# Optimization experiments

Hardware: AMD Instinct MI355X
Metric: run time of the kernel (lower is better)

The kernel has to match this reference:

```python
import jax, jax.numpy as jnp
import numpy as np

D_MODEL, D_FFN, N_LEVELS, N_HEADS, N_POINTS = 256, 1024, 4, 8, 4
B, LQ = 2, 8192
SHAPES = [(128, 128), (64, 64), (32, 32), (16, 16)]  # (H_l, W_l) per level
D_HEAD = D_MODEL // N_HEADS


def setup_inputs() -> dict:
    key = jax.random.key(0)
    ks = jax.random.split(key, 16)
    S = sum(h * w for h, w in SHAPES)

    def lin_w(k, fin, fout):
        s = 1.0 / np.sqrt(fin)
        return jax.random.uniform(k, (fin, fout), jnp.float32, -s, s)

    inp = {
        "tgt": jax.random.normal(ks[0], (B, LQ, D_MODEL), jnp.float32),
        "query_pos": jax.random.normal(ks[1], (B, LQ, D_MODEL), jnp.float32),
        "reference_points": jax.random.uniform(ks[2], (B, LQ, N_LEVELS, 2), jnp.float32),
        "src": jax.random.normal(ks[3], (B, S, D_MODEL), jnp.float32),
        "spatial_shapes": np.array(SHAPES, dtype=np.int64),
        "level_start_index": np.concatenate([[0], np.cumsum([h * w for h, w in SHAPES])[:-1]]).astype(np.int64),
        "W_value": lin_w(ks[4], D_MODEL, D_MODEL),
        "b_value": jnp.zeros((D_MODEL,), jnp.float32),
        "W_off": lin_w(ks[5], D_MODEL, N_HEADS * N_LEVELS * N_POINTS * 2),
        "b_off": 0.5 * jax.random.normal(ks[6], (N_HEADS * N_LEVELS * N_POINTS * 2,), jnp.float32),
        "W_attn": lin_w(ks[7], D_MODEL, N_HEADS * N_LEVELS * N_POINTS),
        "b_attn": jnp.zeros((N_HEADS * N_LEVELS * N_POINTS,), jnp.float32),
        "W_out": lin_w(ks[8], D_MODEL, D_MODEL),
        "b_out": jnp.zeros((D_MODEL,), jnp.float32),
        "ln1_g": jnp.ones((D_MODEL,), jnp.float32),
        "ln1_b": jnp.zeros((D_MODEL,), jnp.float32),
        "W1": lin_w(ks[9], D_MODEL, D_FFN),
        "b1": jnp.zeros((D_FFN,), jnp.float32),
        "W2": lin_w(ks[10], D_FFN, D_MODEL),
        "b2": jnp.zeros((D_MODEL,), jnp.float32),
        "ln3_g": jnp.ones((D_MODEL,), jnp.float32),
        "ln3_b": jnp.zeros((D_MODEL,), jnp.float32),
    }
    return inp


def _layer_norm(x, g, b, eps=1e-5):
    mu = jnp.mean(x, -1, keepdims=True)
    var = jnp.mean((x - mu) ** 2, -1, keepdims=True)
    return (x - mu) * jax.lax.rsqrt(var + eps) * g + b


def _ms_deform_attn(q, reference_points, src, shapes,
                    W_value, b_value, W_off, b_off, W_attn, b_attn, W_out, b_out):
    Bq, Lq, _ = q.shape
    value = (src @ W_value + b_value).reshape(Bq, -1, N_HEADS, D_HEAD)
    value = jnp.transpose(value, (0, 2, 1, 3))  # [B, H, S, Dh]
    off = (q @ W_off + b_off).reshape(Bq, Lq, N_HEADS, N_LEVELS, N_POINTS, 2)
    attn = jax.nn.softmax((q @ W_attn + b_attn).reshape(Bq, Lq, N_HEADS, N_LEVELS * N_POINTS), axis=-1)
    attn = attn.reshape(Bq, Lq, N_HEADS, N_LEVELS, N_POINTS)
    # offset normalizer is (W_l, H_l) per level
    normalizer = jnp.array([[w, h] for h, w in shapes], jnp.float32)
    loc = reference_points[:, :, None, :, None, :] + off / normalizer[None, None, None, :, None, :]

    out = jnp.zeros((Bq, Lq, N_HEADS, D_HEAD), jnp.float32)
    start = 0
    for l, (Hl, Wl) in enumerate(shapes):
        Nl = Hl * Wl
        v_l = value[:, :, start:start + Nl]  # [B, H, Nl, Dh]
        start += Nl
        loc_l = jnp.transpose(loc[:, :, :, l, :, :], (0, 2, 1, 3, 4))  # [B, H, Lq, P, 2]
        # grid_sample (align_corners=False, zero padding) pixel coords
        x = loc_l[..., 0] * Wl - 0.5
        y = loc_l[..., 1] * Hl - 0.5
        x0, y0 = jnp.floor(x), jnp.floor(y)
        wx, wy = x - x0, y - y0
        acc = jnp.zeros((Bq, N_HEADS, Lq, N_POINTS, D_HEAD), jnp.float32)
        for dx, dy, w in ((0, 0, (1 - wx) * (1 - wy)), (1, 0, wx * (1 - wy)),
                          (0, 1, (1 - wx) * wy), (1, 1, wx * wy)):
            xi, yi = x0 + dx, y0 + dy
            valid = (xi >= 0) & (xi < Wl) & (yi >= 0) & (yi < Hl)
            idx = (jnp.clip(yi, 0, Hl - 1) * Wl + jnp.clip(xi, 0, Wl - 1)).astype(jnp.int32)
            g = jnp.take_along_axis(v_l, idx.reshape(Bq, N_HEADS, -1, 1), axis=2)
            g = g.reshape(Bq, N_HEADS, Lq, N_POINTS, D_HEAD)
            acc = acc + jnp.where(valid[..., None], w[..., None] * g, 0.0)
        a = jnp.transpose(attn[:, :, :, l, :], (0, 2, 1, 3))  # [B, H, Lq, P]
        out = out + jnp.einsum('bhqp,bhqpd->bqhd', a, acc)
    return out.reshape(Bq, Lq, D_MODEL) @ W_out + b_out


def reference(tgt, query_pos, reference_points, src, spatial_shapes, level_start_index,
              W_value, b_value, W_off, b_off, W_attn, b_attn, W_out, b_out,
              ln1_g, ln1_b, W1, b1, W2, b2, ln3_g, ln3_b):
    shapes = [(int(h), int(w)) for h, w in np.asarray(spatial_shapes)]
    q = tgt + query_pos  # with_pos_embed
    tgt2 = _ms_deform_attn(q, reference_points, src, shapes,
                           W_value, b_value, W_off, b_off, W_attn, b_attn, W_out, b_out)
    x = _layer_norm(tgt + tgt2, ln1_g, ln1_b)  # dropout = identity (eval)
    ff = jax.nn.relu(x @ W1 + b1) @ W2 + b2
    return _layer_norm(x + ff, ln3_g, ln3_b)
```

## Files before the change

kernel.cpp:

```cpp
#include <hip/hip_runtime.h>
#include <hip/hip_bf16.h>
#include <hip/hip_fp16.h>
#include <math.h>

#define D_MODEL   256
#define D_FFN     1024
#define N_LEVELS  4
#define N_HEADS   8
#define N_POINTS  4
#define BATCH     2
#define LQ        8192
#define S_TOTAL   21760
#define M_Q       (BATCH*LQ)
#define M_V       (BATCH*S_TOTAL)
#define VTILES    (M_V/128)

typedef __attribute__((ext_vector_type(8))) short bf16x8;
typedef __attribute__((ext_vector_type(4))) float floatx4;

struct alignas(8)  bh4 { __hip_bfloat16 a, b, c, d; };
struct alignas(16) bh8 { __hip_bfloat16 v[8]; };

__device__ __forceinline__ void gld_lds16(const void* g, void* l) {
    __builtin_amdgcn_global_load_lds(
        (const __attribute__((address_space(1))) void*)g,
        (__attribute__((address_space(3))) void*)l, 16, 0, 0);
}

__device__ __forceinline__ bh4 pack4(float4 a) {
    return { __float2bfloat16(a.x), __float2bfloat16(a.y),
             __float2bfloat16(a.z), __float2bfloat16(a.w) };
}

template<int BM, int BN, int K>
__device__ __forceinline__ void gemm_core(const __hip_bfloat16* __restrict__ A,
                                          const __hip_bfloat16* __restrict__ Bt,
                                          int row0, int nb0, int lda, int ldb,
                                          short* As, short* Bs,
                                          floatx4 (&acc)[BM/64][BN/16])
{
    constexpr int NT  = BN / 16;
    constexpr int AF  = BM / 64;
    constexpr int BCH = BN / 64;
    constexpr int NIT = K / 32;

    const int tid  = threadIdx.x;
    const int w    = tid >> 6;
    const int lane = tid & 63;
    const int quad = lane >> 4;
    const int l15  = lane & 15;
    const size_t ldaB = (size_t)lda * 2, ldbB = (size_t)ldb * 2;

    const char* gA[AF]; int lA[AF];
#pragma unroll
    for (int i = 0; i < AF; i++) {
        int o = (w * AF + i) * 1024 + lane * 16;
        gA[i] = (const char*)A + (size_t)(row0 + (o >> 6)) * ldaB + (o & 63);
        lA[i] = (w * AF + i) * 512;
    }
    const char* gB[BCH]; int lB[BCH];
#pragma unroll
    for (int j = 0; j < BCH; j++) {
        int o = (w * BCH + j) * 1024 + lane * 16;
        gB[j] = (const char*)Bt + (size_t)(nb0 + (o >> 6)) * ldbB + (o & 63);
        lB[j] = (w * BCH + j) * 512;
    }

#pragma unroll
    for (int i = 0; i < AF; i++)  gld_lds16(gA[i], &As[lA[i]]);
#pragma unroll
    for (int j = 0; j < BCH; j++) gld_lds16(gB[j], &Bs[lB[j]]);

#pragma unroll 8
    for (int it = 0; it < NIT; ++it) {
        __syncthreads();
        const int cb = it & 1;
        if (it + 1 < NIT) {
            const size_t kb = (size_t)(it + 1) * 64;
            const int nb = cb ^ 1;
#pragma unroll
            for (int i = 0; i < AF; i++)  gld_lds16(gA[i] + kb, &As[nb * BM * 32 + lA[i]]);
#pragma unroll
            for (int j = 0; j < BCH; j++) gld_lds16(gB[j] + kb, &Bs[nb * BN * 32 + lB[j]]);
        }
        const short* Ab = &As[cb * BM * 32];
        const short* Bb = &Bs[cb * BN * 32];
        bf16x8 af[AF];
#pragma unroll
        for (int mi = 0; mi < AF; mi++)
            af[mi] = *(const bf16x8*)&Ab[(w * (AF * 16) + mi * 16 + l15) * 32 + quad * 8];
#pragma unroll
        for (int ni = 0; ni < NT; ni++) {
            bf16x8 bfr = *(const bf16x8*)&Bb[(ni * 16 + l15) * 32 + quad * 8];
#pragma unroll
            for (int mi = 0; mi < AF; mi++)
                acc[mi][ni] = __builtin_amdgcn_mfma_f32_16x16x32_bf16(af[mi], bfr, acc[mi][ni], 0, 0, 0);
        }
    }
}

template<int K, bool ADD>
__device__ __forceinline__ void gemm_core_cvtA(const float* __restrict__ Af,
                                               const float* __restrict__ A2f,
                                               const __hip_bfloat16* __restrict__ Bt,
                                               int row0, int nb0, int lda, int ldb,
                                               short* As, short* Bs,
                                               floatx4 (&acc)[2][8])
{
    constexpr int NIT = K / 32;
    const int tid  = threadIdx.x;
    const int w    = tid >> 6;
    const int lane = tid & 63;
    const int quad = lane >> 4;
    const int l15  = lane & 15;

    const int rA  = tid >> 3;
    const int k0  = (tid & 7) * 4;
    const float* gA  = Af + (size_t)(row0 + rA) * lda + k0;
    const float* gA2 = ADD ? (A2f + (size_t)(row0 + rA) * lda + k0) : nullptr;
    const int aoff = rA * 32 + k0;

    const size_t ldbB = (size_t)ldb * 2;
    const char* gB[2]; int lB[2];
#pragma unroll
    for (int j = 0; j < 2; j++) {
        int o = (w * 2 + j) * 1024 + lane * 16;
        gB[j] = (const char*)Bt + (size_t)(nb0 + (o >> 6)) * ldbB + (o & 63);
        lB[j] = (w * 2 + j) * 512;
    }

    float4 fv[4];
    auto loadA = [&](int kt) {
#pragma unroll
        for (int j = 0; j < 4; j++) {
            fv[j] = *(const float4*)(gA + (size_t)(j * 32) * lda + kt);
            if (ADD) {
                float4 t = *(const float4*)(gA2 + (size_t)(j * 32) * lda + kt);
                fv[j].x += t.x; fv[j].y += t.y; fv[j].z += t.z; fv[j].w += t.w;
            }
        }
    };
    auto writeA = [&](short* dstbuf) {
#pragma unroll
        for (int j = 0; j < 4; j++)
            *(bh4*)&dstbuf[j * 1024 + aoff] = pack4(fv[j]);
    };

    loadA(0);
#pragma unroll
    for (int j = 0; j < 2; j++) gld_lds16(gB[j], &Bs[lB[j]]);
    writeA(As);

#pragma unroll 8
    for (int it = 0; it < NIT; ++it) {
        __syncthreads();
        const int cb = it & 1;
        const bool more = (it + 1 < NIT);
        if (more) {
            loadA((it + 1) * 32);
#pragma unroll
            for (int j = 0; j < 2; j++)
                gld_lds16(gB[j] + (size_t)(it + 1) * 64, &Bs[(cb ^ 1) * 128 * 32 + lB[j]]);
        }
        const short* Ab = &As[cb * 128 * 32];
        const short* Bb = &Bs[cb * 128 * 32];
        bf16x8 af[2];
        af[0] = *(const bf16x8*)&Ab[(w * 32      + l15) * 32 + quad * 8];
        af[1] = *(const bf16x8*)&Ab[(w * 32 + 16 + l15) * 32 + quad * 8];
#pragma unroll
        for (int ni = 0; ni < 8; ni++) {
            bf16x8 bfr = *(const bf16x8*)&Bb[(ni * 16 + l15) * 32 + quad * 8];
            acc[0][ni] = __builtin_amdgcn_mfma_f32_16x16x32_bf16(af[0], bfr, acc[0][ni], 0, 0, 0);
            acc[1][ni] = __builtin_amdgcn_mfma_f32_16x16x32_bf16(af[1], bfr, acc[1][ni], 0, 0, 0);
        }
        if (more) writeA(&As[(cb ^ 1) * 128 * 32]);
    }
}

template<int BM, int BN, int K, int EPI>
__global__ __launch_bounds__(256)
void mfma_gemm(const __hip_bfloat16* __restrict__ A,
               const __hip_bfloat16* __restrict__ Bt,
               const float* __restrict__ bias,
               float* __restrict__ outf, __hip_bfloat16* __restrict__ outb,
               int lda, int ldb, int ldOut)
{
    constexpr int NT = BN / 16, AF = BM / 64;
    __shared__ alignas(16) short As[2 * BM * 32];
    __shared__ alignas(16) short Bs[2 * BN * 32];

    const int tid = threadIdx.x, w = tid >> 6, lane = tid & 63;
    const int quad = lane >> 4, l15 = lane & 15;
    const int row0 = blockIdx.x * BM, nb0 = blockIdx.y * BN;

    floatx4 acc[AF][NT];
#pragma unroll
    for (int mi = 0; mi < AF; mi++)
#pragma unroll
        for (int ni = 0; ni < NT; ni++) acc[mi][ni] = (floatx4){0.f, 0.f, 0.f, 0.f};

    gemm_core<BM, BN, K>(A, Bt, row0, nb0, lda, ldb, As, Bs, acc);

    float bias_c[NT];
#pragma unroll
    for (int ni = 0; ni < NT; ni++) bias_c[ni] = bias ? bias[nb0 + ni * 16 + l15] : 0.f;

#pragma unroll
    for (int mi = 0; mi < AF; mi++)
#pragma unroll
        for (int r = 0; r < 4; r++) {
            int row = row0 + w * (AF * 16) + mi * 16 + quad * 4 + r;
            size_t rb = (size_t)row * ldOut + nb0;
#pragma unroll
            for (int ni = 0; ni < NT; ni++) {
                float v = acc[mi][ni][r] + bias_c[ni];
                if (EPI == 2)      outb[rb + ni * 16 + l15] = __float2bfloat16(fmaxf(v, 0.f));
                else if (EPI == 1) outb[rb + ni * 16 + l15] = __float2bfloat16(v);
                else               outf[rb + ni * 16 + l15] = v;
            }
        }
}

__global__ __launch_bounds__(256)
void mfma_gemm_vq(const float* __restrict__ src,
                  const __hip_bfloat16* __restrict__ Wvt,
                  const float* __restrict__ b_value,
                  __hip_bfloat16* __restrict__ valueb,
                  const float* __restrict__ tgt, const float* __restrict__ qpos,
                  const __hip_bfloat16* __restrict__ Woat,
                  const float* __restrict__ b_off, const float* __restrict__ b_attn,
                  float* __restrict__ offb, float* __restrict__ attnb)
{
    __shared__ alignas(16) short As[2 * 128 * 32];
    __shared__ alignas(16) short Bs[2 * 128 * 32];

    const bool isV = blockIdx.x < VTILES;
    if (isV && blockIdx.y == 2) return;

    const int tid = threadIdx.x, w = tid >> 6, lane = tid & 63;
    const int quad = lane >> 4, l15 = lane & 15;
    const int nb0 = blockIdx.y * 128;

    floatx4 acc[2][8];
#pragma unroll
    for (int mi = 0; mi < 2; mi++)
#pragma unroll
        for (int ni = 0; ni < 8; ni++) acc[mi][ni] = (floatx4){0.f, 0.f, 0.f, 0.f};

    if (isV) {
        const int row0 = blockIdx.x * 128;
        gemm_core_cvtA<256, false>(src, nullptr, Wvt, row0, nb0, 256, 256, As, Bs, acc);
        float bias_c[8];
#pragma unroll
        for (int ni = 0; ni < 8; ni++) bias_c[ni] = b_value[nb0 + ni * 16 + l15];
#pragma unroll
        for (int mi = 0; mi < 2; mi++)
#pragma unroll
            for (int r = 0; r < 4; r++) {
                int row = row0 + w * 32 + mi * 16 + quad * 4 + r;
                size_t rb = (size_t)row * 256 + nb0;
#pragma unroll
                for (int ni = 0; ni < 8; ni++)
                    valueb[rb + ni * 16 + l15] = __float2bfloat16(acc[mi][ni][r] + bias_c[ni]);
            }
        return;
    }

    const int row0 = (blockIdx.x - VTILES) * 128;
    gemm_core_cvtA<256, true>(tgt, qpos, Woat, row0, nb0, 256, 256, As, Bs, acc);

    if (blockIdx.y < 2) {
        float bias_c[8];
#pragma unroll
        for (int ni = 0; ni < 8; ni++) bias_c[ni] = b_off[nb0 + ni * 16 + l15];
#pragma unroll
        for (int mi = 0; mi < 2; mi++)
#pragma unroll
            for (int r = 0; r < 4; r++) {
                int row = row0 + w * 32 + mi * 16 + quad * 4 + r;
                size_t rb = (size_t)row * 256 + nb0;
#pragma unroll
                for (int ni = 0; ni < 8; ni++)
                    offb[rb + ni * 16 + l15] = acc[mi][ni][r] + bias_c[ni];
            }
    } else {
        float bias_c[8];
#pragma unroll
        for (int ni = 0; ni < 8; ni++) bias_c[ni] = b_attn[ni * 16 + l15];
#pragma unroll
        for (int mi = 0; mi < 2; mi++)
#pragma unroll
            for (int r = 0; r < 4; r++) {
                int row = row0 + w * 32 + mi * 16 + quad * 4 + r;
                size_t rb = (size_t)row * 128;
#pragma unroll
                for (int ni = 0; ni < 8; ni++) {
                    float v = acc[mi][ni][r] + bias_c[ni];
                    float m = v;
#pragma unroll
                    for (int msk = 1; msk <= 8; msk <<= 1) m = fmaxf(m, __shfl_xor(m, msk));
                    float e = __expf(v - m);
                    float ssum = e;
#pragma unroll
                    for (int msk = 1; msk <= 8; msk <<= 1) ssum += __shfl_xor(ssum, msk);
                    attnb[rb + ni * 16 + l15] = e / ssum;
                }
            }
    }
}

template<bool B1>
__global__ __launch_bounds__(256)
void ln_kernel(const float* __restrict__ in1f, const __hip_bfloat16* __restrict__ in1b,
               const float* __restrict__ resid, const float* __restrict__ bias,
               const float* __restrict__ g, const float* __restrict__ b,
               float* __restrict__ outf, __hip_bfloat16* __restrict__ outb)
{
    const int row  = blockIdx.x * 4 + (threadIdx.x >> 6);
    const int lane = threadIdx.x & 63;
    const size_t rb = (size_t)row * 256 + lane * 4;

    float4 v = *(const float4*)(resid + rb);
    if (B1) {
        bh4 a = *(const bh4*)(in1b + rb);
        v.x += __bfloat162float(a.a); v.y += __bfloat162float(a.b);
        v.z += __bfloat162float(a.c); v.w += __bfloat162float(a.d);
    } else {
        float4 a = *(const float4*)(in1f + rb);
        v.x += a.x; v.y += a.y; v.z += a.z; v.w += a.w;
    }
    if (bias) {
        float4 c = *(const float4*)(bias + lane * 4);
        v.x += c.x; v.y += c.y; v.z += c.z; v.w += c.w;
    }
    float s  = v.x + v.y + v.z + v.w;
    float sq = v.x * v.x + v.y * v.y + v.z * v.z + v.w * v.w;
#pragma unroll
    for (int msk = 1; msk <= 32; msk <<= 1) {
        s += __shfl_xor(s, msk); sq += __shfl_xor(sq, msk);
    }
    float mean = s * (1.f / 256.f);
    float var  = sq * (1.f / 256.f) - mean * mean;
    float rstd = rsqrtf(var + 1e-5f);
    float4 gg = *(const float4*)(g + lane * 4);
    float4 bb = *(const float4*)(b + lane * 4);
    float4 o;
    o.x = (v.x - mean) * rstd * gg.x + bb.x;
    o.y = (v.y - mean) * rstd * gg.y + bb.y;
    o.z = (v.z - mean) * rstd * gg.z + bb.z;
    o.w = (v.w - mean) * rstd * gg.w + bb.w;
    *(float4*)(outf + rb) = o;
    if (outb)
        *(bh4*)(outb + rb) = { __float2bfloat16(o.x), __float2bfloat16(o.y),
                               __float2bfloat16(o.z), __float2bfloat16(o.w) };
}

__global__ __launch_bounds__(256)
void prep_kernel(const float* w0, const float* w1, const float* w2,
                 const float* w3, const float* w4, const float* w5,
                 __hip_bfloat16* o0, __hip_bfloat16* o1, __hip_bfloat16* o2,
                 __hip_bfloat16* o3, __hip_bfloat16* o4, __hip_bfloat16* o5)
{
    int t = blockIdx.x;
    const float* s; __hip_bfloat16* dst; int Kd, Nd, tl;
    if      (t < 64)  { s = w0; dst = o0; Kd = 256;  Nd = 256;  tl = t; }
    else if (t < 128) { s = w1; dst = o1; Kd = 256;  Nd = 256;  tl = t - 64; }
    else if (t < 160) { s = w2; dst = o2; Kd = 256;  Nd = 128;  tl = t - 128; }
    else if (t < 224) { s = w3; dst = o3; Kd = 256;  Nd = 256;  tl = t - 160; }
    else if (t < 480) { s = w4; dst = o4; Kd = 256;  Nd = 1024; tl = t - 224; }
    else              { s = w5; dst = o5; Kd = 1024; Nd = 256;  tl = t - 480; }
    int ntn = Nd >> 5;
    int kt = tl / ntn, nt = tl - kt * ntn;
    __shared__ float T[32][33];
    int tx = threadIdx.x & 31, ty = threadIdx.x >> 5;
#pragma unroll
    for (int i = 0; i < 4; i++) {
        int k = kt * 32 + ty + i * 8;
        T[tx][ty + i * 8] = s[(size_t)k * Nd + nt * 32 + tx];
    }
    __syncthreads();
#pragma unroll
    for (int i = 0; i < 4; i++) {
        int n = nt * 32 + ty + i * 8;
        dst[(size_t)n * Kd + kt * 32 + tx] = __float2bfloat16(T[ty + i * 8][tx]);
    }
}

#define QB 8
__global__ __launch_bounds__(256, 4)
void sample_kernel(const float* __restrict__ refp, const float* __restrict__ offb,
                   const float* __restrict__ attn,
                   const __hip_bfloat16* __restrict__ value,
                   __hip_bfloat16* __restrict__ tgt2)
{
    __shared__ unsigned spk[64 * 65];

    const int q0  = blockIdx.x * QB;
    const int tid = threadIdx.x;

#pragma unroll
    for (int k = 0; k < 4; k++) {
        const int it = tid + k * 256;
        const int ql = it >> 7, h = (it >> 4) & 7, lp = it & 15;
        const int l = lp >> 2, p = lp & 3;
        const int q = q0 + ql, b = q >> 13;
        const int Wl = 128 >> l;
        const int LST = (l == 0) ? 0 : (l == 1) ? 16384 : (l == 2) ? 20480 : 21504;

        const float rx = refp[((size_t)q * N_LEVELS + l) * 2 + 0];
        const float ry = refp[((size_t)q * N_LEVELS + l) * 2 + 1];
        const float ox = offb[(size_t)q * 256 + h * 32 + l * 8 + p * 2 + 0];
        const float oy = offb[(size_t)q * 256 + h * 32 + l * 8 + p * 2 + 1];
        const float a  = attn[(size_t)q * 128 + h * 16 + lp];

        const float x = rx * Wl - 0.5f + ox;
        const float y = ry * Wl - 0.5f + oy;
        const float x0f = floorf(x), y0f = floorf(y);
        const float wx = x - x0f, wy = y - y0f;
        const int ix = (int)x0f, iy = (int)y0f;
        const int base = b * S_TOTAL + LST;
        const int g = ql * 8 + h;
        const float cw[4] = {(1.f - wx) * (1.f - wy) * a, wx * (1.f - wy) * a,
                             (1.f - wx) * wy * a,         wx * wy * a};
#pragma unroll
        for (int c = 0; c < 4; c++) {
            const int xi = ix + (c & 1), yi = iy + (c >> 1);
            const bool valid = ((unsigned)xi < (unsigned)Wl) && ((unsigned)yi < (unsigned)Wl);
            const unsigned pix = valid ? (unsigned)(base + yi * Wl + xi) : (unsigned)base;
            const __half hw = __float2half(valid ? cw[c] : 0.f);
            spk[(lp * 4 + c) * 65 + g] = (pix << 16) | (unsigned)__half_as_ushort(hw);
        }
    }
    __syncthreads();

    const int ql = tid >> 5, h = (tid >> 2) & 7, d4 = tid & 3;
    const int q = q0 + ql, g = ql * 8 + h;
    const int c0 = h * 32 + d4 * 8;
    const char* vb = (const char*)value + (size_t)c0 * 2;

    float ac[8] = {0.f, 0.f, 0.f, 0.f, 0.f, 0.f, 0.f, 0.f};
#pragma unroll
    for (int ch = 0; ch < 4; ch++) {
        unsigned us[16];
#pragma unroll
        for (int j = 0; j < 16; j++) us[j] = spk[(ch * 16 + j) * 65 + g];
        uint4 rv[16];
#pragma unroll
        for (int j = 0; j < 16; j++)
            rv[j] = *(const uint4*)(vb + ((size_t)(us[j] >> 16) << 9));
#pragma unroll
        for (int j = 0; j < 16; j++) {
            float wv = __half2float(__ushort_as_half((unsigned short)(us[j] & 0xffffu)));
            ac[0] += wv * __uint_as_float(rv[j].x << 16);
            ac[1] += wv * __uint_as_float(rv[j].x & 0xffff0000u);
            ac[2] += wv * __uint_as_float(rv[j].y << 16);
            ac[3] += wv * __uint_as_float(rv[j].y & 0xffff0000u);
            ac[4] += wv * __uint_as_float(rv[j].z << 16);
            ac[5] += wv * __uint_as_float(rv[j].z & 0xffff0000u);
            ac[6] += wv * __uint_as_float(rv[j].w << 16);
            ac[7] += wv * __uint_as_float(rv[j].w & 0xffff0000u);
        }
    }
    bh8 o;
#pragma unroll
    for (int i = 0; i < 8; i++) o.v[i] = __float2bfloat16(ac[i]);
    *(bh8*)(tgt2 + (size_t)q * 256 + c0) = o;
}

extern "C" void kernel_launch(void* const* d_in, const int* in_sizes, int n_in,
                              void* d_out, int out_size, void* d_ws, size_t ws_size,
                              hipStream_t stream) {
    const float* tgt     = (const float*)d_in[0];
    const float* qpos    = (const float*)d_in[1];
    const float* refp    = (const float*)d_in[2];
    const float* src     = (const float*)d_in[3];
    const float* W_value = (const float*)d_in[6];
    const float* b_value = (const float*)d_in[7];
    const float* W_off   = (const float*)d_in[8];
    const float* b_off   = (const float*)d_in[9];
    const float* W_attn  = (const float*)d_in[10];
    const float* b_attn  = (const float*)d_in[11];
    const float* W_out   = (const float*)d_in[12];
    const float* b_out   = (const float*)d_in[13];
    const float* ln1_g   = (const float*)d_in[14];
    const float* ln1_b   = (const float*)d_in[15];
    const float* W1      = (const float*)d_in[16];
    const float* b1      = (const float*)d_in[17];
    const float* W2      = (const float*)d_in[18];
    const float* b2      = (const float*)d_in[19];
    const float* ln3_g   = (const float*)d_in[20];
    const float* ln3_b   = (const float*)d_in[21];
    float* out = (float*)d_out;

    char* p = (char*)d_ws;
    auto nxt = [&](size_t b) { char* r = p; p += (b + 255) & ~(size_t)255; return r; };
    __hip_bfloat16* Wvt    = (__hip_bfloat16*)nxt((size_t)256 * 256 * 2);
    __hip_bfloat16* Woat   = (__hip_bfloat16*)nxt((size_t)384 * 256 * 2);
    __hip_bfloat16* Woutt  = (__hip_bfloat16*)nxt((size_t)256 * 256 * 2);
    __hip_bfloat16* W1t    = (__hip_bfloat16*)nxt((size_t)1024 * 256 * 2);
    __hip_bfloat16* W2t    = (__hip_bfloat16*)nxt((size_t)256 * 1024 * 2);
    __hip_bfloat16* valueb = (__hip_bfloat16*)nxt((size_t)M_V * 256 * 2);
    float*          offb   = (float*)nxt((size_t)M_Q * 256 * 4);
    float*          attnb  = (float*)nxt((size_t)M_Q * 128 * 4);
    __hip_bfloat16* tgt2b  = (__hip_bfloat16*)nxt((size_t)M_Q * 256 * 2);
    __hip_bfloat16* t2ob   = (__hip_bfloat16*)nxt((size_t)M_Q * 256 * 2);
    float*          x      = (float*)nxt((size_t)M_Q * 256 * 4);
    __hip_bfloat16* xb     = (__hip_bfloat16*)nxt((size_t)M_Q * 256 * 2);
    __hip_bfloat16* hb     = (__hip_bfloat16*)nxt((size_t)M_Q * 1024 * 2);
    float* f2o = (float*)valueb;

    dim3 blk(256);

    prep_kernel<<<dim3(736), blk, 0, stream>>>(
        W_value, W_off, W_attn, W_out, W1, W2,
        Wvt, Woat, Woat + 256 * 256, Woutt, W1t, W2t);

    mfma_gemm_vq<<<dim3(VTILES + M_Q / 128, 3), blk, 0, stream>>>(
        src, Wvt, b_value, valueb, tgt, qpos, Woat, b_off, b_attn, offb, attnb);

    sample_kernel<<<dim3(M_Q / QB), blk, 0, stream>>>(refp, offb, attnb, valueb, tgt2b);

    mfma_gemm<64, 128, 256, 1><<<dim3(M_Q / 64, 2), blk, 0, stream>>>(
        tgt2b, Woutt, b_out, nullptr, t2ob, 256, 256, 256);

    ln_kernel<true><<<dim3(M_Q / 4), blk, 0, stream>>>(
        nullptr, t2ob, tgt, nullptr, ln1_g, ln1_b, x, xb);

    mfma_gemm<128, 128, 256, 2><<<dim3(M_Q / 128, 8), blk, 0, stream>>>(
        xb, W1t, b1, nullptr, hb, 256, 256, 1024);

    mfma_gemm<64, 128, 1024, 0><<<dim3(M_Q / 64, 2), blk, 0, stream>>>(
        hb, W2t, b2, f2o, nullptr, 1024, 1024, 256);

    ln_kernel<false><<<dim3(M_Q / 4), blk, 0, stream>>>(
        f2o, nullptr, x, nullptr, ln3_g, ln3_b, out, nullptr);
}
```

Before: 299.6 us.

## Replace LDS-staged double-buffered GEMM cores with direct global-to-register MFMA loads

New measurement: 418.5 us. +39.7%, slower.

```diff
diff --git a/kernel.cpp b/kernel.cpp
--- a/kernel.cpp
+++ b/kernel.cpp
@@ -21,163 +21,73 @@
 struct alignas(8)  bh4 { __hip_bfloat16 a, b, c, d; };
 struct alignas(16) bh8 { __hip_bfloat16 v[8]; };
 
-__device__ __forceinline__ void gld_lds16(const void* g, void* l) {
-    __builtin_amdgcn_global_load_lds(
-        (const __attribute__((address_space(1))) void*)g,
-        (__attribute__((address_space(3))) void*)l, 16, 0, 0);
-}
-
-__device__ __forceinline__ bh4 pack4(float4 a) {
-    return { __float2bfloat16(a.x), __float2bfloat16(a.y),
-             __float2bfloat16(a.z), __float2bfloat16(a.w) };
-}
-
-template<int BM, int BN, int K>
-__device__ __forceinline__ void gemm_core(const __hip_bfloat16* __restrict__ A,
-                                          const __hip_bfloat16* __restrict__ Bt,
-                                          int row0, int nb0, int lda, int ldb,
-                                          short* As, short* Bs,
-                                          floatx4 (&acc)[BM/64][BN/16])
-{
-    constexpr int NT  = BN / 16;
-    constexpr int AF  = BM / 64;
-    constexpr int BCH = BN / 64;
-    constexpr int NIT = K / 32;
-
+__device__ __forceinline__ bf16x8 pack8(float4 a, float4 b) {
+    bh8 o;
+    o.v[0] = __float2bfloat16(a.x); o.v[1] = __float2bfloat16(a.y);
+    o.v[2] = __float2bfloat16(a.z); o.v[3] = __float2bfloat16(a.w);
+    o.v[4] = __float2bfloat16(b.x); o.v[5] = __float2bfloat16(b.y);
+    o.v[6] = __float2bfloat16(b.z); o.v[7] = __float2bfloat16(b.w);
+    return *(bf16x8*)&o;
+}
+
+template<int AF, int NT, int K, int F32A>
+__device__ __forceinline__ void gemm_direct(const char* __restrict__ Ab,
+                                            const float* __restrict__ A2,
+                                            const __hip_bfloat16* __restrict__ Bt,
+                                            int row0, int nb0, int lda, int ldb,
+                                            floatx4 (&acc)[AF][NT])
+{
     const int tid  = threadIdx.x;
     const int w    = tid >> 6;
     const int lane = tid & 63;
     const int quad = lane >> 4;
     const int l15  = lane & 15;
-    const size_t ldaB = (size_t)lda * 2, ldbB = (size_t)ldb * 2;
-
-    const char* gA[AF]; int lA[AF];
-#pragma unroll
-    for (int i = 0; i < AF; i++) {
-        int o = (w * AF + i) * 1024 + lane * 16;
-        gA[i] = (const char*)A + (size_t)(row0 + (o >> 6)) * ldaB + (o & 63);
-        lA[i] = (w * AF + i) * 512;
-    }
-    const char* gB[BCH]; int lB[BCH];
-#pragma unroll
-    for (int j = 0; j < BCH; j++) {
-        int o = (w * BCH + j) * 1024 + lane * 16;
-        gB[j] = (const char*)Bt + (size_t)(nb0 + (o >> 6)) * ldbB + (o & 63);
-        lB[j] = (w * BCH + j) * 512;
-    }
-
-#pragma unroll
-    for (int i = 0; i < AF; i++)  gld_lds16(gA[i], &As[lA[i]]);
-#pragma unroll
-    for (int j = 0; j < BCH; j++) gld_lds16(gB[j], &Bs[lB[j]]);
+
+    const char* Ap[AF]; const float* A2p[AF];
+#pragma unroll
+    for (int mi = 0; mi < AF; mi++) {
+        const int r = row0 + w * (AF * 16) + mi * 16 + l15;
+        Ap[mi] = Ab + ((size_t)r * lda + quad * 8) * (F32A ? 4 : 2);
+        A2p[mi] = (F32A == 2) ? (A2 + (size_t)r * lda + quad * 8) : nullptr;
+    }
+    const char* Bp[NT];
+#pragma unroll
+    for (int ni = 0; ni < NT; ni++)
+        Bp[ni] = (const char*)(Bt + (size_t)(nb0 + ni * 16 + l15) * ldb + quad * 8);
 
 #pragma unroll 8
-    for (int it = 0; it < NIT; ++it) {
-        __syncthreads();
-        const int cb = it & 1;
-        if (it + 1 < NIT) {
-            const size_t kb = (size_t)(it + 1) * 64;
-            const int nb = cb ^ 1;
-#pragma unroll
-            for (int i = 0; i < AF; i++)  gld_lds16(gA[i] + kb, &As[nb * BM * 32 + lA[i]]);
-#pragma unroll
-            for (int j = 0; j < BCH; j++) gld_lds16(gB[j] + kb, &Bs[nb * BN * 32 + lB[j]]);
-        }
-        const short* Ab = &As[cb * BM * 32];
-        const short* Bb = &Bs[cb * BN * 32];
+    for (int it = 0; it < K / 32; ++it) {
+        const int kt = it * 32;
         bf16x8 af[AF];
 #pragma unroll
-        for (int mi = 0; mi < AF; mi++)
-            af[mi] = *(const bf16x8*)&Ab[(w * (AF * 16) + mi * 16 + l15) * 32 + quad * 8];
-#pragma unroll
-        for (int ni = 0; ni < NT; ni++) {
-            bf16x8 bfr = *(const bf16x8*)&Bb[(ni * 16 + l15) * 32 + quad * 8];
-#pragma unroll
-            for (int mi = 0; mi < AF; mi++)
-                acc[mi][ni] = __builtin_amdgcn_mfma_f32_16x16x32_bf16(af[mi], bfr, acc[mi][ni], 0, 0, 0);
-        }
-    }
-}
-
-template<int K, bool ADD>
-__device__ __forceinline__ void gemm_core_cvtA(const float* __restrict__ Af,
-                                               const float* __restrict__ A2f,
-                                               const __hip_bfloat16* __restrict__ Bt,
-                                               int row0, int nb0, int lda, int ldb,
-                                               short* As, short* Bs,
-                                               floatx4 (&acc)[2][8])
-{
-    constexpr int NIT = K / 32;
-    const int tid  = threadIdx.x;
-    const int w    = tid >> 6;
-    const int lane = tid & 63;
-    const int quad = lane >> 4;
-    const int l15  = lane & 15;
-
-    const int rA  = tid >> 3;
-    const int k0  = (tid & 7) * 4;
-    const float* gA  = Af + (size_t)(row0 + rA) * lda + k0;
-    const float* gA2 = ADD ? (A2f + (size_t)(row0 + rA) * lda + k0) : nullptr;
-    const int aoff = rA * 32 + k0;
-
-    const size_t ldbB = (size_t)ldb * 2;
-    const char* gB[2]; int lB[2];
-#pragma unroll
-    for (int j = 0; j < 2; j++) {
-        int o = (w * 2 + j) * 1024 + lane * 16;
-        gB[j] = (const char*)Bt + (size_t)(nb0 + (o >> 6)) * ldbB + (o & 63);
-        lB[j] = (w * 2 + j) * 512;
-    }
-
-    float4 fv[4];
-    auto loadA = [&](int kt) {
-#pragma unroll
-        for (int j = 0; j < 4; j++) {
-            fv[j] = *(const float4*)(gA + (size_t)(j * 32) * lda + kt);
-            if (ADD) {
-                float4 t = *(const float4*)(gA2 + (size_t)(j * 32) * lda + kt);
-                fv[j].x += t.x; fv[j].y += t.y; fv[j].z += t.z; fv[j].w += t.w;
+        for (int mi = 0; mi < AF; mi++) {
+            if (F32A == 0) {
+                af[mi] = *(const bf16x8*)(Ap[mi] + (size_t)kt * 2);
+            } else {
+                float4 f0 = *(const float4*)(Ap[mi] + (size_t)kt * 4);
+                float4 f1 = *(const float4*)(Ap[mi] + (size_t)kt * 4 + 16);
+                if (F32A == 2) {
+                    float4 g0 = *(const float4*)(A2p[mi] + kt);
+                    float4 g1 = *(const float4*)(A2p[mi] + kt + 4);
+                    f0.x += g0.x; f0.y += g0.y; f0.z += g0.z; f0.w += g0.w;
+                    f1.x += g1.x; f1.y += g1.y; f1.z += g1.z; f1.w += g1.w;
+                }
+                af[mi] = pack8(f0, f1);
             }
         }
-    };
-    auto writeA = [&](short* dstbuf) {
-#pragma unroll
-        for (int j = 0; j < 4; j++)
-            *(bh4*)&dstbuf[j * 1024 + aoff] = pack4(fv[j]);
-    };
-
-    loadA(0);
-#pragma unroll
-    for (int j = 0; j < 2; j++) gld_lds16(gB[j], &Bs[lB[j]]);
-    writeA(As);
-
-#pragma unroll 8
-    for (int it = 0; it < NIT; ++it) {
-        __syncthreads();
-        const int cb = it & 1;
-        const bool more = (it + 1 < NIT);
-        if (more) {
-            loadA((it + 1) * 32);
-#pragma unroll
-            for (int j = 0; j < 2; j++)
-                gld_lds16(gB[j] + (size_t)(it + 1) * 64, &Bs[(cb ^ 1) * 128 * 32 + lB[j]]);
-        }
-        const short* Ab = &As[cb * 128 * 32];
-        const short* Bb = &Bs[cb * 128 * 32];
-        bf16x8 af[2];
-        af[0] = *(const bf16x8*)&Ab[(w * 32      + l15) * 32 + quad * 8];
-        af[1] = *(const bf16x8*)&Ab[(w * 32 + 16 + l15) * 32 + quad * 8];
-#pragma unroll
-        for (int ni = 0; ni < 8; ni++) {
-            bf16x8 bfr = *(const bf16x8*)&Bb[(ni * 16 + l15) * 32 + quad * 8];
-            acc[0][ni] = __builtin_amdgcn_mfma_f32_16x16x32_bf16(af[0], bfr, acc[0][ni], 0, 0, 0);
-            acc[1][ni] = __builtin_amdgcn_mfma_f32_16x16x32_bf16(af[1], bfr, acc[1][ni], 0, 0, 0);
-        }
-        if (more) writeA(&As[(cb ^ 1) * 128 * 32]);
-    }
-}
-
-template<int BM, int BN, int K, int EPI>
+        bf16x8 bfr[NT];
+#pragma unroll
+        for (int ni = 0; ni < NT; ni++)
+            bfr[ni] = *(const bf16x8*)(Bp[ni] + (size_t)kt * 2);
+#pragma unroll
+        for (int ni = 0; ni < NT; ni++)
+#pragma unroll
+            for (int mi = 0; mi < AF; mi++)
+                acc[mi][ni] = __builtin_amdgcn_mfma_f32_16x16x32_bf16(af[mi], bfr[ni], acc[mi][ni], 0, 0, 0);
+    }
+}
+
+template<int AF, int NT, int K, int EPI>
 __global__ __launch_bounds__(256)
 void mfma_gemm(const __hip_bfloat16* __restrict__ A,
                const __hip_bfloat16* __restrict__ Bt,
@@ -185,13 +95,9 @@
                float* __restrict__ outf, __hip_bfloat16* __restrict__ outb,
                int lda, int ldb, int ldOut)
 {
-    constexpr int NT = BN / 16, AF = BM / 64;
-    __shared__ alignas(16) short As[2 * BM * 32];
-    __shared__ alignas(16) short Bs[2 * BN * 32];
-
     const int tid = threadIdx.x, w = tid >> 6, lane = tid & 63;
     const int quad = lane >> 4, l15 = lane & 15;
-    const int row0 = blockIdx.x * BM, nb0 = blockIdx.y * BN;
+    const int row0 = blockIdx.x * (AF * 64), nb0 = blockIdx.y * (NT * 16);
 
     floatx4 acc[AF][NT];
 #pragma unroll
@@ -199,7 +105,7 @@
 #pragma unroll
         for (int ni = 0; ni < NT; ni++) acc[mi][ni] = (floatx4){0.f, 0.f, 0.f, 0.f};
 
-    gemm_core<BM, BN, K>(A, Bt, row0, nb0, lda, ldb, As, Bs, acc);
+    gemm_direct<AF, NT, K, 0>((const char*)A, nullptr, Bt, row0, nb0, lda, ldb, acc);
 
     float bias_c[NT];
 #pragma unroll
@@ -231,9 +137,6 @@
                   const float* __restrict__ b_off, const float* __restrict__ b_attn,
                   float* __restrict__ offb, float* __restrict__ attnb)
 {
-    __shared__ alignas(16) short As[2 * 128 * 32];
-    __shared__ alignas(16) short Bs[2 * 128 * 32];
-
     const bool isV = blockIdx.x < VTILES;
     if (isV && blockIdx.y == 2) return;
 
@@ -249,7 +152,7 @@
 
     if (isV) {
         const int row0 = blockIdx.x * 128;
-        gemm_core_cvtA<256, false>(src, nullptr, Wvt, row0, nb0, 256, 256, As, Bs, acc);
+        gemm_direct<2, 8, 256, 1>((const char*)src, nullptr, Wvt, row0, nb0, 256, 256, acc);
         float bias_c[8];
 #pragma unroll
         for (int ni = 0; ni < 8; ni++) bias_c[ni] = b_value[nb0 + ni * 16 + l15];
@@ -267,7 +170,7 @@
     }
 
     const int row0 = (blockIdx.x - VTILES) * 128;
-    gemm_core_cvtA<256, true>(tgt, qpos, Woat, row0, nb0, 256, 256, As, Bs, acc);
+    gemm_direct<2, 8, 256, 2>((const char*)tgt, qpos, Woat, row0, nb0, 256, 256, acc);
 
     if (blockIdx.y < 2) {
         float bias_c[8];
@@ -520,16 +423,16 @@
 
     sample_kernel<<<dim3(M_Q / QB), blk, 0, stream>>>(refp, offb, attnb, valueb, tgt2b);
 
-    mfma_gemm<64, 128, 256, 1><<<dim3(M_Q / 64, 2), blk, 0, stream>>>(
+    mfma_gemm<1, 4, 256, 1><<<dim3(M_Q / 64, 4), blk, 0, stream>>>(
         tgt2b, Woutt, b_out, nullptr, t2ob, 256, 256, 256);
 
     ln_kernel<true><<<dim3(M_Q / 4), blk, 0, stream>>>(
         nullptr, t2ob, tgt, nullptr, ln1_g, ln1_b, x, xb);
 
-    mfma_gemm<128, 128, 256, 2><<<dim3(M_Q / 128, 8), blk, 0, stream>>>(
+    mfma_gemm<2, 8, 256, 2><<<dim3(M_Q / 128, 8), blk, 0, stream>>>(
         xb, W1t, b1, nullptr, hb, 256, 256, 1024);
 
-    mfma_gemm<64, 128, 1024, 0><<<dim3(M_Q / 64, 2), blk, 0, stream>>>(
+    mfma_gemm<1, 4, 1024, 0><<<dim3(M_Q / 64, 4), blk, 0, stream>>>(
         hb, W2t, b2, f2o, nullptr, 1024, 1024, 256);
 
     ln_kernel<false><<<dim3(M_Q / 4), blk, 0, stream>>>(
```
